# Kernel optimization log

Measured on AMD Instinct MI355X. Metric: run time of the kernel, lower is better.

The kernel has to match this reference:

```python
import math
import jax, jax.numpy as jnp
import numpy as np

TOP_K = 2
N_EXP = 8
TRAIN_CAPACITY = 1.25
MIN_CAPACITY = 4


def _capacity(num_tokens):
    cap = math.floor(TOP_K * TRAIN_CAPACITY * num_tokens / N_EXP)
    cap += cap % 2
    return max(cap, MIN_CAPACITY)


def _router(x, w_g):
    B, T, D = x.shape
    N = B * T
    C = _capacity(N)  # static: depends only on shapes

    logits = jnp.einsum('btd,ed->bte', x, w_g)            # [B,T,E]
    _, top_idx = jax.lax.top_k(logits, TOP_K)             # [B,T,K]
    probs = jax.nn.softmax(logits, axis=-1).reshape(N, N_EXP)  # [N,E]
    idx = top_idx.reshape(N, TOP_K)                       # [N,K]

    # one-hot expert mask, laid out [K, N, E] as in the torch code
    exp_mask = jax.nn.one_hot(idx, N_EXP, dtype=jnp.int32)      # [N,K,E]
    exp_mask = jnp.transpose(exp_mask, (1, 0, 2))               # [K,N,E]

    # position of each routed token within its expert's queue
    rank = jnp.cumsum(exp_mask.reshape(TOP_K * N, N_EXP), axis=0)
    rank = rank.reshape(TOP_K, N, N_EXP) - 1                    # [K,N,E]

    exp_mask = exp_mask * (rank < C).astype(jnp.int32)          # drop over-capacity
    used_capacity = jnp.sum(exp_mask, axis=(0, 1))              # [E]
    rank_sel = jnp.sum(exp_mask * rank, axis=-1)                # [K,N] int

    idx_kn = jnp.transpose(idx)                                 # [K,N]
    keep = jnp.take_along_axis(exp_mask, idx_kn[:, :, None], axis=2)[..., 0]  # [K,N]
    p_sel = jnp.transpose(jnp.take_along_axis(probs, idx, axis=1))            # [K,N]
    w = keep.astype(probs.dtype) * p_sel                        # [K,N]

    # cb_weight[n, e, c] = sum_k exp_weights[k,n,e] * one_hot(rank_sel)[k,n,c]
    # implemented as a direct scatter-add instead of materializing the
    # O(K*N*E*C) outer product (dropped tokens contribute weight 0).
    tok = jnp.arange(N)
    cb_weight = jnp.zeros((N, N_EXP, C), probs.dtype)
    cb_weight = cb_weight.at[tok[None, :], idx_kn, rank_sel].add(w)
    sec_mask = cb_weight != 0
    return used_capacity, cb_weight, sec_mask


def setup_inputs() -> dict:
    key = jax.random.key(0)
    kx, kw = jax.random.split(key)
    x = jax.random.normal(kx, (2, 2048, 1024), dtype=jnp.float32)
    w_g = jax.random.normal(kw, (8, 1024), dtype=jnp.float32) * 0.02
    return {"x": x, "w_g": w_g}


def reference(x, w_g):
    return _router(x, w_g)
```

## Files before the change

kernel.cpp:

```cpp
#include <hip/hip_runtime.h>

#define N_TOK 4096
#define DIM   1024
#define NE    8
#define CAP   1280
#define EC    (NE * CAP)
#define NEC   (N_TOK * EC)
#define OUT_ELEMS (8 + 2 * NEC)
#define OUT_VEC4  (OUT_ELEMS / 4)

__global__ __launch_bounds__(256) void k_logits(const float* __restrict__ x,
                                                const float* __restrict__ wg,
                                                int* __restrict__ top_idx,
                                                float* __restrict__ top_p) {
    __shared__ float swg[NE * DIM];
    const float4* wg4 = (const float4*)wg;
    float4* swg4 = (float4*)swg;
#pragma unroll
    for (int i = 0; i < 8; ++i) {
        int t = i * 256 + threadIdx.x;
        swg4[t] = wg4[t];
    }
    __syncthreads();

    const int wave = threadIdx.x >> 6;
    const int lane = threadIdx.x & 63;
    const int token = blockIdx.x * 4 + wave;

    const float4* x4 = (const float4*)(x + (size_t)token * DIM);
    float acc[NE];
#pragma unroll
    for (int e = 0; e < NE; ++e) acc[e] = 0.f;

#pragma unroll
    for (int c = 0; c < 4; ++c) {
        float4 xv = x4[c * 64 + lane];
#pragma unroll
        for (int e = 0; e < NE; ++e) {
            float4 wv = swg4[e * 256 + c * 64 + lane];
            acc[e] += xv.x * wv.x + xv.y * wv.y + xv.z * wv.z + xv.w * wv.w;
        }
    }
#pragma unroll
    for (int e = 0; e < NE; ++e) {
        float v = acc[e];
#pragma unroll
        for (int off = 32; off > 0; off >>= 1)
            v += __shfl_xor(v, off, 64);
        acc[e] = v;
    }

    if (lane == 0) {
        float m = acc[0];
#pragma unroll
        for (int e = 1; e < NE; ++e) m = fmaxf(m, acc[e]);
        float pe[NE];
        float s = 0.f;
#pragma unroll
        for (int e = 0; e < NE; ++e) { pe[e] = expf(acc[e] - m); s += pe[e]; }
        float inv = 1.f / s;

        int i1 = 0; float v1 = acc[0];
#pragma unroll
        for (int e = 1; e < NE; ++e) if (acc[e] > v1) { v1 = acc[e]; i1 = e; }
        int i2 = (i1 == 0) ? 1 : 0; float v2 = acc[i2];
#pragma unroll
        for (int e = 0; e < NE; ++e)
            if (e != i1 && acc[e] > v2) { v2 = acc[e]; i2 = e; }

        top_idx[token]         = i1;
        top_idx[N_TOK + token] = i2;
        top_p[token]           = pe[i1] * inv;
        top_p[N_TOK + token]   = pe[i2] * inv;
    }
}

__global__ __launch_bounds__(64) void k_rank(const int* __restrict__ top_idx,
                                             int* __restrict__ dest,
                                             float* __restrict__ used) {
    __shared__ int se[2 * N_TOK];
    const int lane = threadIdx.x;
    const int4* ti4 = (const int4*)top_idx;
    int4* se4 = (int4*)se;
#pragma unroll
    for (int i = 0; i < 32; ++i)
        se4[i * 64 + lane] = ti4[i * 64 + lane];
    __syncthreads();

    int cnt[NE];
#pragma unroll
    for (int e = 0; e < NE; ++e) cnt[e] = 0;
    const int base = lane * 128;
    for (int jj = 0; jj < 128; ++jj) cnt[se[base + jj]]++;

    int excl[NE], tot[NE];
#pragma unroll
    for (int e = 0; e < NE; ++e) {
        int v = cnt[e];
        int inc = v;
#pragma unroll
        for (int off = 1; off < 64; off <<= 1) {
            int u = __shfl_up(inc, off, 64);
            if (lane >= off) inc += u;
        }
        excl[e] = inc - v;
        tot[e] = __shfl(inc, 63, 64);
    }
    if (lane < NE) used[lane] = (float)min(tot[lane], CAP);

    int run[NE];
#pragma unroll
    for (int e = 0; e < NE; ++e) run[e] = excl[e];
    for (int jj = 0; jj < 128; ++jj) {
        int j = base + jj;
        int e = se[j];
        int r = run[e]++;
        int n = j & (N_TOK - 1);
        dest[j] = (r < CAP) ? (n * EC + e * CAP + r) : -1;
    }
}

__global__ __launch_bounds__(256) void k_fill(float4* __restrict__ out, int n4) {
    int i = blockIdx.x * blockDim.x + threadIdx.x;
    const int stride = gridDim.x * blockDim.x;
    const float4 z = {0.f, 0.f, 0.f, 0.f};
    for (; i < n4; i += stride) out[i] = z;
}

__global__ __launch_bounds__(256) void k_scatter(const int* __restrict__ dest,
                                                 const float* __restrict__ top_p,
                                                 const float* __restrict__ used,
                                                 float* __restrict__ out) {
    int j = blockIdx.x * blockDim.x + threadIdx.x;
    if (j < NE) out[j] = used[j];
    if (j < 2 * N_TOK) {
        int d = dest[j];
        if (d >= 0) {
            out[(size_t)8 + d] = top_p[j];
            out[(size_t)8 + NEC + d] = 1.0f;
        }
    }
}

extern "C" void kernel_launch(void* const* d_in, const int* in_sizes, int n_in,
                              void* d_out, int out_size, void* d_ws, size_t ws_size,
                              hipStream_t stream) {
    const float* x  = (const float*)d_in[0];
    const float* wg = (const float*)d_in[1];
    float* out = (float*)d_out;
    char* ws = (char*)d_ws;

    int*   top_idx = (int*)(ws);
    float* top_p   = (float*)(ws + 32768);
    int*   dest    = (int*)(ws + 65536);
    float* used    = (float*)(ws + 98304);

    k_logits<<<N_TOK / 4, 256, 0, stream>>>(x, wg, top_idx, top_p);
    k_rank<<<1, 64, 0, stream>>>(top_idx, dest, used);
    k_fill<<<4096, 256, 0, stream>>>((float4*)out, OUT_VEC4);
    k_scatter<<<(2 * N_TOK + 255) / 256, 256, 0, stream>>>(dest, top_p, used, out);
}
```

Baseline: 393.6 us.

## Fuse zero-fill and scatter into one dense per-token output writer

The rank kernel now builds a per-slot table (expert×capacity) holding the owning token and its weight, with unused slots set to -1. A new output kernel, launched with one block per token, writes that token's full cb_weight and mask rows in a single dense float4 pass by comparing each slot's owner to the token. This replaces the separate full-buffer zero fill plus random scatter, removing one kernel launch and the scattered writes. In exchange every block re-reads the whole slot table (tok+weight) from cache, so total read traffic matches the output size.

```diff
diff --git a/kernel.cpp b/kernel.cpp
--- a/kernel.cpp
+++ b/kernel.cpp
@@ -5,9 +5,8 @@
 #define NE    8
 #define CAP   1280
 #define EC    (NE * CAP)
-#define NEC   (N_TOK * EC)
-#define OUT_ELEMS (8 + 2 * NEC)
-#define OUT_VEC4  (OUT_ELEMS / 4)
+#define EC4   (EC / 4)
+#define NEC   ((size_t)N_TOK * EC)
 
 __global__ __launch_bounds__(256) void k_logits(const float* __restrict__ x,
                                                 const float* __restrict__ wg,
@@ -76,7 +75,9 @@
 }
 
 __global__ __launch_bounds__(64) void k_rank(const int* __restrict__ top_idx,
-                                             int* __restrict__ dest,
+                                             const float* __restrict__ top_p,
+                                             int* __restrict__ slot_tok,
+                                             float* __restrict__ slot_w,
                                              float* __restrict__ used) {
     __shared__ int se[2 * N_TOK];
     const int lane = threadIdx.x;
@@ -115,30 +116,44 @@
         int j = base + jj;
         int e = se[j];
         int r = run[e]++;
-        int n = j & (N_TOK - 1);
-        dest[j] = (r < CAP) ? (n * EC + e * CAP + r) : -1;
+        if (r < CAP) {
+            slot_tok[e * CAP + r] = j & (N_TOK - 1);
+            slot_w[e * CAP + r]   = top_p[j];
+        }
+    }
+#pragma unroll
+    for (int e = 0; e < NE; ++e) {
+        int start = min(tot[e], CAP);
+        for (int s = start + lane; s < CAP; s += 64)
+            slot_tok[e * CAP + s] = -1;
     }
 }
 
-__global__ __launch_bounds__(256) void k_fill(float4* __restrict__ out, int n4) {
-    int i = blockIdx.x * blockDim.x + threadIdx.x;
-    const int stride = gridDim.x * blockDim.x;
-    const float4 z = {0.f, 0.f, 0.f, 0.f};
-    for (; i < n4; i += stride) out[i] = z;
-}
+__global__ __launch_bounds__(256) void k_out(const int* __restrict__ slot_tok,
+                                             const float* __restrict__ slot_w,
+                                             const float* __restrict__ used,
+                                             float* __restrict__ out) {
+    const int n = blockIdx.x;
+    const int t = threadIdx.x;
+    if (n == 0 && t < NE) out[t] = used[t];
 
-__global__ __launch_bounds__(256) void k_scatter(const int* __restrict__ dest,
-                                                 const float* __restrict__ top_p,
-                                                 const float* __restrict__ used,
-                                                 float* __restrict__ out) {
-    int j = blockIdx.x * blockDim.x + threadIdx.x;
-    if (j < NE) out[j] = used[j];
-    if (j < 2 * N_TOK) {
-        int d = dest[j];
-        if (d >= 0) {
-            out[(size_t)8 + d] = top_p[j];
-            out[(size_t)8 + NEC + d] = 1.0f;
-        }
+    float4* cb = (float4*)(out + 8 + (size_t)n * EC);
+    float4* mk = (float4*)(out + 8 + NEC + (size_t)n * EC);
+    const int4* st4 = (const int4*)slot_tok;
+    const float4* sw4 = (const float4*)slot_w;
+
+#pragma unroll
+    for (int i = 0; i < EC4 / 256; ++i) {
+        int v = t + 256 * i;
+        int4 tk = st4[v];
+        float4 w = sw4[v];
+        float4 c, m;
+        c.x = (tk.x == n) ? w.x : 0.f;  m.x = (tk.x == n) ? 1.f : 0.f;
+        c.y = (tk.y == n) ? w.y : 0.f;  m.y = (tk.y == n) ? 1.f : 0.f;
+        c.z = (tk.z == n) ? w.z : 0.f;  m.z = (tk.z == n) ? 1.f : 0.f;
+        c.w = (tk.w == n) ? w.w : 0.f;  m.w = (tk.w == n) ? 1.f : 0.f;
+        cb[v] = c;
+        mk[v] = m;
     }
 }
 
@@ -150,13 +165,13 @@
     float* out = (float*)d_out;
     char* ws = (char*)d_ws;
 
-    int*   top_idx = (int*)(ws);
-    float* top_p   = (float*)(ws + 32768);
-    int*   dest    = (int*)(ws + 65536);
-    float* used    = (float*)(ws + 98304);
+    int*   top_idx  = (int*)(ws);
+    float* top_p    = (float*)(ws + 32768);
+    int*   slot_tok = (int*)(ws + 65536);
+    float* slot_w   = (float*)(ws + 106496);
+    float* used     = (float*)(ws + 147456);
 
     k_logits<<<N_TOK / 4, 256, 0, stream>>>(x, wg, top_idx, top_p);
-    k_rank<<<1, 64, 0, stream>>>(top_idx, dest, used);
-    k_fill<<<4096, 256, 0, stream>>>((float4*)out, OUT_VEC4);
-    k_scatter<<<(2 * N_TOK + 255) / 256, 256, 0, stream>>>(dest, top_p, used, out);
+    k_rank<<<1, 64, 0, stream>>>(top_idx, top_p, slot_tok, slot_w, used);
+    k_out<<<N_TOK, 256, 0, stream>>>(slot_tok, slot_w, used, out);
 }
```

After: 391.9 us. About the same (-0.4%).
